# Kernel optimization log

Measured on AMD Instinct MI355X. Metric: run time of the kernel, lower is better.

Reference implementation:

```python
import jax, jax.numpy as jnp
import numpy as np
import math

# ---------- helpers ----------

def conv(x, w, b=None, pad=1):
    y = jax.lax.conv_general_dilated(x, w, (1, 1), [(pad, pad), (pad, pad)],
                                     dimension_numbers=('NCHW', 'OIHW', 'NCHW'))
    return y if b is None else y + b[None, :, None, None]


def bn(x, g, b, m, v, eps=1e-5):
    scale = (g / jnp.sqrt(v + eps))[None, :, None, None]
    return (x - m[None, :, None, None]) * scale + b[None, :, None, None]


def _interp(x, axis, out_size):
    # bilinear resize along one axis with align_corners=True semantics
    n = x.shape[axis]
    c = jnp.arange(out_size, dtype=jnp.float32) * (n - 1) / (out_size - 1)
    lo = jnp.floor(c).astype(jnp.int32)
    hi = jnp.minimum(lo + 1, n - 1)
    w = c - lo
    xl = jnp.take(x, lo, axis=axis)
    xh = jnp.take(x, hi, axis=axis)
    wshape = [1] * x.ndim
    wshape[axis] = out_size
    w = w.reshape(wshape)
    return xl * (1.0 - w) + xh * w


def upsample2x(x):
    B, C, H, W = x.shape
    return _interp(_interp(x, 2, 2 * H), 3, 2 * W)


def haar_dwt2d(x):
    # single-level orthonormal haar DWT; equivalent to the per-(b,c) dwt2d loop,
    # vectorized over batch and channel via strided slicing
    a = x[..., 0::2, 0::2]
    b = x[..., 0::2, 1::2]
    c = x[..., 1::2, 0::2]
    d = x[..., 1::2, 1::2]
    LL = (a + b + c + d) * 0.5
    LH = (-a - b + c + d) * 0.5  # horizontal detail (row differences)
    HL = (-a + b - c + d) * 0.5  # vertical detail (col differences)
    HH = (a - b - c + d) * 0.5
    return LL, LH, HL, HH


def gabor_kernels(k=7, sigma=4.0, lambd=10.0, gamma=0.5, psi=0.0):
    thetas = jnp.array([0.0, math.pi / 4, math.pi / 2, 3 * math.pi / 4], dtype=jnp.float32)
    r = jnp.arange(-(k // 2), k // 2 + 1, dtype=jnp.float32)
    y, x = jnp.meshgrid(r, r, indexing='ij')

    def one(theta):
        xt = x * jnp.cos(theta) + y * jnp.sin(theta)
        yt = -x * jnp.sin(theta) + y * jnp.cos(theta)
        return jnp.exp(-0.5 * (xt ** 2 / sigma ** 2 + yt ** 2 / (sigma / gamma) ** 2)) \
               * jnp.cos(2.0 * math.pi * xt / lambd + psi)

    return jax.vmap(one)(thetas)[:, None]  # [4,1,k,k]


def cbam(x, fc1_w, fc2_w, sp_w):
    avg = x.mean(axis=(2, 3))
    mx = x.max(axis=(2, 3))
    mlp = lambda v: jax.nn.relu(v @ fc1_w.T) @ fc2_w.T
    ca = jax.nn.sigmoid(mlp(avg) + mlp(mx))[:, :, None, None]
    x = x * ca
    sp = jnp.concatenate([x.mean(axis=1, keepdims=True), x.max(axis=1, keepdims=True)], axis=1)
    sa = jax.nn.sigmoid(conv(sp, sp_w, pad=3))
    return x * sa


# ---------- inputs ----------

def setup_inputs() -> dict:
    B, Cin, Cout, H, W = 16, 64, 64, 128, 128
    Cr = Cout // 16
    ks = jax.random.split(jax.random.key(0), 32)
    p = lambda k, s, sc=0.05: jax.random.normal(k, s, dtype=jnp.float32) * sc
    g = lambda k, c: 1.0 + 0.1 * jax.random.normal(k, (c,), dtype=jnp.float32)
    return {
        'x': jax.random.normal(ks[0], (B, Cin, H, W), dtype=jnp.float32),
        'conv_in_w': p(ks[1], (Cout, Cin, 3, 3)),
        'bn1_g': g(ks[2], Cout), 'bn1_b': p(ks[3], (Cout,)),
        'bn1_m': p(ks[4], (Cout,)), 'bn1_v': jax.random.uniform(ks[5], (Cout,), minval=0.5, maxval=1.5),
        'down1_w': p(ks[6], (1, Cout, 3, 3)), 'down1_b': p(ks[7], (1,)),
        'down2_w': p(ks[8], (1, Cout, 3, 3)), 'down2_b': p(ks[9], (1,)),
        'wt_w': p(ks[10], (1, 1, 3, 3)), 'wt_b': p(ks[11], (1,)),
        'edge_w': p(ks[12], (Cout, 1, 3, 3)), 'edge_b': p(ks[13], (Cout,)),
        'up_w': p(ks[14], (Cout, 2, 3, 3)),
        'bn2_g': g(ks[15], Cout), 'bn2_b': p(ks[16], (Cout,)),
        'bn2_m': p(ks[17], (Cout,)), 'bn2_v': jax.random.uniform(ks[18], (Cout,), minval=0.5, maxval=1.5),
        'combine_w': p(ks[19], (Cout, 2 * Cout, 3, 3)), 'combine_b': p(ks[20], (Cout,)),
        'cbam_fc1_w': p(ks[21], (Cr, Cout)), 'cbam_fc2_w': p(ks[22], (Cout, Cr)),
        'cbam_sp_w': p(ks[23], (1, 2, 7, 7)),
        'out_w': p(ks[24], (Cout, Cout, 3, 3)),
        'bn3_g': g(ks[25], Cout), 'bn3_b': p(ks[26], (Cout,)),
        'bn3_m': p(ks[27], (Cout,)), 'bn3_v': jax.random.uniform(ks[28], (Cout,), minval=0.5, maxval=1.5),
    }


def reference(x, conv_in_w, bn1_g, bn1_b, bn1_m, bn1_v, down1_w, down1_b,
              down2_w, down2_b, wt_w, wt_b, edge_w, edge_b, up_w,
              bn2_g, bn2_b, bn2_m, bn2_v, combine_w, combine_b,
              cbam_fc1_w, cbam_fc2_w, cbam_sp_w, out_w,
              bn3_g, bn3_b, bn3_m, bn3_v):
    x1 = jax.nn.relu(bn(conv(x, conv_in_w), bn1_g, bn1_b, bn1_m, bn1_v))   # BasicConv2d
    X = upsample2x(x1)                                                      # [B,C,2H,2W]
    x_in = conv(x1, down1_w, down1_b)                                       # [B,1,H,W]
    X_in = conv(X, down2_w, down2_b)                                        # [B,1,2H,2W]
    cA, cH, cV, cD = haar_dwt2d(X_in)                                       # [B,1,H,W] each
    edge = conv(jnp.abs(cH) + jnp.abs(cV) + jnp.abs(cD), edge_w, edge_b)    # [B,C,H,W]
    gk = gabor_kernels()                                                    # all 4 thetas in one conv
    gab = jax.nn.sigmoid(conv(x_in, gk, pad=3).mean(axis=1, keepdims=True))
    wt = conv(cA, wt_w, wt_b)
    fusion = jax.nn.relu(bn(conv(jnp.concatenate([wt, gab], axis=1), up_w),
                            bn2_g, bn2_b, bn2_m, bn2_v))
    fusion = conv(jnp.concatenate([fusion, edge * (x1 + 1.0)], axis=1), combine_w, combine_b)
    att = cbam(fusion, cbam_fc1_w, cbam_fc2_w, cbam_sp_w)
    return jax.nn.relu(bn(conv(att, out_w), bn3_g, bn3_b, bn3_m, bn3_v))
```

## Files before the change

kernel.cpp:

```cpp
#include <hip/hip_runtime.h>
#include <math.h>

#define HWc 16384
#define Wd 128
#define Hd 128

typedef __attribute__((ext_vector_type(8))) _Float16 half8;
typedef __attribute__((ext_vector_type(4))) _Float16 half4;
typedef __attribute__((ext_vector_type(4))) float f32x4;

#define GLDS16(gp, lp) __builtin_amdgcn_global_load_lds( \
    (const __attribute__((address_space(1))) void*)(gp), \
    (__attribute__((address_space(3))) void*)(lp), 16, 0, 0)

__global__ void prep_all_kernel(const float* __restrict__ w_in,
                                const float* __restrict__ w_out,
                                const float* __restrict__ w_comb,
                                _Float16* __restrict__ wf_in,
                                _Float16* __restrict__ wf_out,
                                _Float16* __restrict__ wf_comb)
{
    int bid = blockIdx.x;
    const float* w; _Float16* wf; int cin; int idx;
    if (bid < 144)      { w = w_in;   wf = wf_in;   cin = 64;  idx = bid * 256 + threadIdx.x; }
    else if (bid < 288) { w = w_out;  wf = wf_out;  cin = 64;  idx = (bid - 144) * 256 + threadIdx.x; }
    else                { w = w_comb; wf = wf_comb; cin = 128; idx = (bid - 288) * 256 + threadIdx.x; }
    int total = cin * 576;
    if (idx >= total) return;
    int KC = cin >> 5;
    int j = idx & 7;
    int lane = (idx >> 3) & 63;
    int rest = idx >> 9;
    int ot = rest & 3;
    int rest2 = rest >> 2;
    int kc = rest2 % KC;
    int t = rest2 / KC;
    int oc = ot * 16 + (lane & 15);
    int ci = kc * 32 + ((lane >> 4) << 3) + j;
    wf[idx] = (_Float16)w[((size_t)oc * cin + ci) * 9 + t];
}

__global__ __launch_bounds__(256) void pack8_kernel(const float* __restrict__ in,
                                                    _Float16* __restrict__ outp)
{
    int idx = blockIdx.x * 256 + threadIdx.x;
    int b = idx >> 14, p = idx & 16383;
    #pragma unroll
    for (int g = 0; g < 8; g++) {
        half8 v;
        #pragma unroll
        for (int k = 0; k < 8; k++)
            v[k] = (_Float16)in[((size_t)b * 64 + g * 8 + k) * HWc + p];
        *(half8*)&outp[(((size_t)b * 8 + g) * HWc + p) * 8] = v;
    }
}

__global__ __launch_bounds__(64, 3) void mfma_conv64_kernel(
    const _Float16* __restrict__ inp8, const _Float16* __restrict__ wf,
    const float* __restrict__ bng, const float* __restrict__ bnb,
    const float* __restrict__ bnm, const float* __restrict__ bnv,
    _Float16* __restrict__ outp8, float* __restrict__ out32)
{
    __shared__ __align__(16) _Float16 slds[6912];
    __shared__ float sc[64], sh[64];
    int lane = threadIdx.x;
    int b = blockIdx.y;
    int tileid = blockIdx.x;
    int ty = tileid >> 3, tx = tileid & 7;
    int h0 = ty * 4 - 1, w0 = tx * 16 - 1;
    const _Float16* ib = inp8 + (size_t)b * 8 * HWc * 8;
    bool interior = (ty >= 1 && ty <= 30 && tx >= 1 && tx <= 6);
    if (interior) {
        #pragma unroll
        for (int it = 0; it < 14; it++) {
            int i = it * 64 + lane;
            if (i < 864) {
                int g = i / 108;
                int rem = i - g * 108;
                int y = rem / 18, x = rem - (rem / 18) * 18;
                int p = (h0 + y) * Wd + (w0 + x);
                GLDS16(&ib[((size_t)g * HWc + p) * 8], &slds[it * 512]);
            }
        }
    } else {
        #pragma unroll
        for (int it = 0; it < 14; it++) {
            int i = it * 64 + lane;
            if (i < 864) {
                int g = i / 108;
                int rem = i - g * 108;
                int y = rem / 18, x = rem - (rem / 18) * 18;
                int hh = h0 + y, ww = w0 + x;
                if (hh >= 0 && hh < Hd && ww >= 0 && ww < Wd) {
                    int p = hh * Wd + ww;
                    GLDS16(&ib[((size_t)g * HWc + p) * 8], &slds[it * 512]);
                } else {
                    half8 hz;
                    #pragma unroll
                    for (int k = 0; k < 8; k++) hz[k] = (_Float16)0.f;
                    *(half8*)&slds[i * 8] = hz;
                }
            }
        }
    }
    {
        float inv = rsqrtf(bnv[lane] + 1e-5f);
        float s = bng[lane] * inv;
        sc[lane] = s;
        sh[lane] = bnb[lane] - bnm[lane] * s;
    }
    __syncthreads();
    int lq = lane >> 4, ln = lane & 15;
    f32x4 acc[4][4];
    #pragma unroll
    for (int r = 0; r < 4; r++)
        #pragma unroll
        for (int ot = 0; ot < 4; ot++)
            #pragma unroll
            for (int q = 0; q < 4; q++) acc[r][ot][q] = 0.f;

    for (int t = 0; t < 9; t++) {
        int dy = t / 3, dx = t - (t / 3) * 3;
        #pragma unroll
        for (int kc = 0; kc < 2; kc++) {
            half8 bf[4];
            #pragma unroll
            for (int r = 0; r < 4; r++) {
                int off = (((kc * 4 + lq) * 108) + (r + dy) * 18 + (ln + dx)) * 8;
                bf[r] = *(const half8*)&slds[off];
            }
            #pragma unroll
            for (int ot = 0; ot < 4; ot++) {
                half8 af = *(const half8*)(wf + (size_t)(((t * 2 + kc) * 4 + ot) * 64 + lane) * 8);
                #pragma unroll
                for (int r = 0; r < 4; r++)
                    acc[r][ot] = __builtin_amdgcn_mfma_f32_16x16x32_f16(af, bf[r], acc[r][ot], 0, 0, 0);
            }
        }
    }
    #pragma unroll
    for (int r = 0; r < 4; r++) {
        int yy = ty * 4 + r;
        int p = yy * Wd + tx * 16 + ln;
        #pragma unroll
        for (int ot = 0; ot < 4; ot++) {
            int g4 = ot * 4 + lq;
            if (out32) {
                #pragma unroll
                for (int reg = 0; reg < 4; reg++) {
                    int oc = g4 * 4 + reg;
                    float v = fmaf(acc[r][ot][reg], sc[oc], sh[oc]);
                    out32[((size_t)b * 64 + oc) * HWc + p] = fmaxf(v, 0.f);
                }
            } else {
                half4 hv;
                #pragma unroll
                for (int reg = 0; reg < 4; reg++) {
                    int oc = g4 * 4 + reg;
                    float v = fmaf(acc[r][ot][reg], sc[oc], sh[oc]);
                    hv[reg] = (_Float16)fmaxf(v, 0.f);
                }
                *(half4*)&outp8[(((size_t)b * 8 + (g4 >> 1)) * HWc + p) * 8 + (g4 & 1) * 4] = hv;
            }
        }
    }
}

__global__ __launch_bounds__(64, 3) void mfma_combine_kernel(
    const _Float16* __restrict__ f1p, const _Float16* __restrict__ emod,
    const _Float16* __restrict__ wf, const float* __restrict__ cb,
    _Float16* __restrict__ outp8)
{
    __shared__ __align__(16) _Float16 slds[6912];
    __shared__ float cbl[64];
    int lane = threadIdx.x;
    int b = blockIdx.y;
    int tileid = blockIdx.x;
    int ty = tileid >> 3, tx = tileid & 7;
    int h0 = ty * 4 - 1, w0 = tx * 16 - 1;
    int lq = lane >> 4, ln = lane & 15;
    bool interior = (ty >= 1 && ty <= 30 && tx >= 1 && tx <= 6);
    f32x4 acc[4][4];
    #pragma unroll
    for (int r = 0; r < 4; r++)
        #pragma unroll
        for (int ot = 0; ot < 4; ot++)
            #pragma unroll
            for (int q = 0; q < 4; q++) acc[r][ot][q] = 0.f;

    const _Float16* f1b = f1p + (size_t)b * 8 * HWc * 8;
    const _Float16* emb = emod + (size_t)b * 8 * HWc * 8;
    bool cbl_done = false;
    for (int h = 0; h < 2; h++) {
        const _Float16* src = (h == 0) ? f1b : emb;
        if (h) __syncthreads();
        if (interior) {
            #pragma unroll
            for (int it = 0; it < 14; it++) {
                int i = it * 64 + lane;
                if (i < 864) {
                    int g = i / 108;
                    int rem = i - g * 108;
                    int y = rem / 18, x = rem - (rem / 18) * 18;
                    int p = (h0 + y) * Wd + (w0 + x);
                    GLDS16(&src[((size_t)g * HWc + p) * 8], &slds[it * 512]);
                }
            }
        } else {
            #pragma unroll
            for (int it = 0; it < 14; it++) {
                int i = it * 64 + lane;
                if (i < 864) {
                    int g = i / 108;
                    int rem = i - g * 108;
                    int y = rem / 18, x = rem - (rem / 18) * 18;
                    int hh = h0 + y, ww = w0 + x;
                    if (hh >= 0 && hh < Hd && ww >= 0 && ww < Wd) {
                        int p = hh * Wd + ww;
                        GLDS16(&src[((size_t)g * HWc + p) * 8], &slds[it * 512]);
                    } else {
                        half8 hz;
                        #pragma unroll
                        for (int k = 0; k < 8; k++) hz[k] = (_Float16)0.f;
                        *(half8*)&slds[i * 8] = hz;
                    }
                }
            }
        }
        if (!cbl_done) { cbl[lane] = cb[lane]; cbl_done = true; }
        __syncthreads();
        for (int t = 0; t < 9; t++) {
            int dy = t / 3, dx = t - (t / 3) * 3;
            #pragma unroll
            for (int kc = 0; kc < 2; kc++) {
                int kcg = h * 2 + kc;
                half8 bf[4];
                #pragma unroll
                for (int r = 0; r < 4; r++) {
                    int off = (((kc * 4 + lq) * 108) + (r + dy) * 18 + (ln + dx)) * 8;
                    bf[r] = *(const half8*)&slds[off];
                }
                #pragma unroll
                for (int ot = 0; ot < 4; ot++) {
                    half8 af = *(const half8*)(wf + (size_t)(((t * 4 + kcg) * 4 + ot) * 64 + lane) * 8);
                    #pragma unroll
                    for (int r = 0; r < 4; r++)
                        acc[r][ot] = __builtin_amdgcn_mfma_f32_16x16x32_f16(af, bf[r], acc[r][ot], 0, 0, 0);
                }
            }
        }
    }
    #pragma unroll
    for (int r = 0; r < 4; r++) {
        int yy = ty * 4 + r;
        int p = yy * Wd + tx * 16 + ln;
        #pragma unroll
        for (int ot = 0; ot < 4; ot++) {
            int g4 = ot * 4 + lq;
            half4 hv;
            #pragma unroll
            for (int reg = 0; reg < 4; reg++) {
                int oc = g4 * 4 + reg;
                hv[reg] = (_Float16)(acc[r][ot][reg] + cbl[oc]);
            }
            *(half4*)&outp8[(((size_t)b * 8 + (g4 >> 1)) * HWc + p) * 8 + (g4 & 1) * 4] = hv;
        }
    }
}

__global__ __launch_bounds__(256) void edgemul_kernel(const float* __restrict__ E,
    const _Float16* __restrict__ x1p, const float* __restrict__ edge_w,
    const float* __restrict__ edge_b, _Float16* __restrict__ emod)
{
    __shared__ float ew[576];
    __shared__ float ebl[64];
    int tid = threadIdx.x;
    for (int i = tid; i < 576; i += 256) ew[i] = edge_w[i];
    if (tid < 64) ebl[tid] = edge_b[tid];
    __syncthreads();
    int idx = blockIdx.x * 256 + tid;
    int b = idx >> 14, p = idx & 16383;
    int i = p >> 7, j = p & 127;
    const float* ep = E + (size_t)b * HWc;
    float e[9];
    #pragma unroll
    for (int tt = 0; tt < 9; tt++) {
        int ii = i - 1 + tt / 3, jj = j - 1 + tt % 3;
        e[tt] = (ii >= 0 && ii < Hd && jj >= 0 && jj < Wd) ? ep[ii * Wd + jj] : 0.f;
    }
    const _Float16* xb = x1p + (size_t)b * 8 * HWc * 8;
    _Float16* ob = emod + (size_t)b * 8 * HWc * 8;
    for (int g = 0; g < 8; g++) {
        half8 v = *(const half8*)&xb[((size_t)g * HWc + p) * 8];
        half8 hv;
        #pragma unroll
        for (int k = 0; k < 8; k++) {
            int cc = g * 8 + k;
            float ec = ebl[cc];
            #pragma unroll
            for (int tt = 0; tt < 9; tt++) ec = fmaf(ew[cc * 9 + tt], e[tt], ec);
            float xv = (float)v[k];
            hv[k] = (_Float16)(ec * (xv + 1.0f));
        }
        *(half8*)&ob[((size_t)g * HWc + p) * 8] = hv;
    }
}

__global__ __launch_bounds__(256) void conv3x3_bn_kernel(
    const float* __restrict__ in, const float* __restrict__ wgt,
    const float* __restrict__ bng, const float* __restrict__ bnb,
    const float* __restrict__ bnm, const float* __restrict__ bnv,
    _Float16* __restrict__ outp8, int cin)
{
    __shared__ float tile[18*18];
    __shared__ float wl[576];
    __shared__ float sc[64], sh[64];
    int tid = threadIdx.x;
    int tileid = blockIdx.x; int b = blockIdx.y;
    int th = tileid >> 3, tw = tileid & 7;
    int h0 = th*16 - 1, w0 = tw*16 - 1;
    if (tid < 64) {
        float inv = rsqrtf(bnv[tid] + 1e-5f);
        float s = bng[tid]*inv;
        sc[tid] = s;
        sh[tid] = bnb[tid] - bnm[tid]*s;
    }
    float acc[64];
    #pragma unroll
    for (int i=0;i<64;i++) acc[i]=0.f;
    int py = tid>>4, px = tid&15;
    for (int ci=0; ci<cin; ci++){
        __syncthreads();
        const float* inp = in + ((size_t)b*cin + ci)*HWc;
        for (int i = tid; i < 324; i += 256) {
            int y=i/18, x=i%18; int hh=h0+y, ww=w0+x;
            tile[i] = (hh>=0&&hh<Hd&&ww>=0&&ww<Wd) ? inp[hh*Wd+ww] : 0.f;
        }
        for (int i = tid; i < 576; i += 256) {
            int oc = i/9, t = i - oc*9;
            wl[i] = wgt[((size_t)oc*cin + ci)*9 + t];
        }
        __syncthreads();
        float v[9];
        #pragma unroll
        for (int dy=0;dy<3;dy++)
            #pragma unroll
            for (int dx=0;dx<3;dx++)
                v[dy*3+dx] = tile[(py+dy)*18 + px+dx];
        #pragma unroll
        for (int oc=0;oc<64;oc++){
            float a = acc[oc];
            #pragma unroll
            for (int t=0;t<9;t++) a = fmaf(wl[oc*9+t], v[t], a);
            acc[oc]=a;
        }
    }
    int hh = h0+1+py, ww = w0+1+px;
    int p = hh*Wd + ww;
    #pragma unroll
    for (int g=0; g<8; g++){
        half8 hv;
        #pragma unroll
        for (int k=0; k<8; k++){
            int oc = g*8+k;
            float y = fmaf(acc[oc], sc[oc], sh[oc]);
            hv[k] = (_Float16)fmaxf(y, 0.f);
        }
        *(half8*)&outp8[(((size_t)b*8+g)*HWc + p)*8] = hv;
    }
}

__global__ __launch_bounds__(256) void zmaps_kernel(const _Float16* __restrict__ x1p,
    const float* __restrict__ w2, const float* __restrict__ w1,
    float* __restrict__ z, float* __restrict__ z1)
{
    int idx = blockIdx.x*256 + threadIdx.x;
    int b = idx >> 14; int p = idx & 16383;
    const _Float16* xb = x1p + (size_t)b*8*HWc*8;
    float a2[9], a1[9];
    #pragma unroll
    for (int t=0;t<9;t++){ a2[t]=0.f; a1[t]=0.f; }
    for (int g=0; g<8; g++){
        half8 v = *(const half8*)&xb[((size_t)g*HWc + p)*8];
        #pragma unroll
        for (int k=0;k<8;k++){
            int c = g*8+k;
            float val = (float)v[k];
            #pragma unroll
            for (int t=0;t<9;t++){
                a2[t] = fmaf(w2[c*9+t], val, a2[t]);
                a1[t] = fmaf(w1[c*9+t], val, a1[t]);
            }
        }
    }
    #pragma unroll
    for (int t=0;t<9;t++){
        z [((size_t)b*9+t)*HWc + p] = a2[t];
        z1[((size_t)b*9+t)*HWc + p] = a1[t];
    }
}

__global__ __launch_bounds__(256) void xin_kernel(const float* __restrict__ z1,
    const float* __restrict__ b1p, float* __restrict__ xin)
{
    int idx = blockIdx.x*256+threadIdx.x;
    int b=idx>>14; int p=idx&16383;
    int i=p>>7, j=p&127;
    float acc = b1p[0];
    #pragma unroll
    for (int t=0;t<9;t++){
        int ii=i+t/3-1, jj=j+t%3-1;
        if (ii>=0&&ii<Hd&&jj>=0&&jj<Wd)
            acc += z1[((size_t)b*9+t)*HWc + ii*Wd+jj];
    }
    xin[idx]=acc;
}

__global__ __launch_bounds__(256) void dwt_kernel(const float* __restrict__ z,
    const float* __restrict__ b2p, float* __restrict__ cA, float* __restrict__ Eo)
{
    int idx = blockIdx.x*256 + threadIdx.x;
    int b = idx >> 14; int p = idx & 16383;
    int u = p >> 7, v = p & 127;
    float b2 = b2p[0];
    int rlo[4], rhi[4]; float rf[4]; bool rv[4];
    int clo[4], chi[4]; float cf[4]; bool cvv[4];
    #pragma unroll
    for (int k=0;k<4;k++){
        int r = 2*u - 1 + k;
        rv[k] = (r>=0 && r<256);
        int rr = rv[k] ? r : 0;
        float cc = ((float)rr * 127.0f) / 255.0f;
        int lo = (int)cc;
        rlo[k]=lo; rhi[k]=min(lo+1,127); rf[k]=cc-(float)lo;
        int s = 2*v - 1 + k;
        cvv[k] = (s>=0 && s<256);
        int ss = cvv[k] ? s : 0;
        float c2 = ((float)ss * 127.0f) / 255.0f;
        int lo2=(int)c2;
        clo[k]=lo2; chi[k]=min(lo2+1,127); cf[k]=c2-(float)lo2;
    }
    float Xin[4] = {b2,b2,b2,b2};
    #pragma unroll
    for (int t=0;t<9;t++){
        int dy=t/3, dx=t%3;
        const float* zp = z + ((size_t)b*9 + t)*HWc;
        #pragma unroll
        for (int e=0;e<4;e++){
            int ey=e>>1, ex=e&1;
            int k=ey+dy, l=ex+dx;
            if (rv[k] && cvv[l]){
                const float* row0 = zp + rlo[k]*Wd;
                const float* row1 = zp + rhi[k]*Wd;
                float v00=row0[clo[l]], v01=row0[chi[l]];
                float v10=row1[clo[l]], v11=row1[chi[l]];
                float fc_=cf[l], fr_=rf[k];
                float top = v00*(1.0f-fc_) + v01*fc_;
                float bot = v10*(1.0f-fc_) + v11*fc_;
                Xin[e] += top*(1.0f-fr_) + bot*fr_;
            }
        }
    }
    float a=Xin[0], bb=Xin[1], c_=Xin[2], d_=Xin[3];
    float LL=0.5f*( a+bb+c_+d_);
    float LH=0.5f*(-a-bb+c_+d_);
    float HL=0.5f*(-a+bb-c_+d_);
    float HH=0.5f*( a-bb-c_+d_);
    cA[(size_t)b*HWc + p] = LL;
    Eo[(size_t)b*HWc + p] = fabsf(LH)+fabsf(HL)+fabsf(HH);
}

__global__ __launch_bounds__(256) void wtgab_kernel(const float* __restrict__ cA,
    const float* __restrict__ xin, const float* __restrict__ wtw, const float* __restrict__ wtb,
    float* __restrict__ wtgab)
{
    __shared__ float gm[49];
    int tid=threadIdx.x;
    if (tid<49){
        int ky=tid/7, kx=tid%7;
        float yy=(float)(ky-3), xx=(float)(kx-3);
        float s=0.f;
        for (int t=0;t<4;t++){
            float theta = (float)t * 0.7853981633974483f;
            float ct=cosf(theta), st=sinf(theta);
            float xt = xx*ct + yy*st;
            float yt = -xx*st + yy*ct;
            s += expf(-0.5f*(xt*xt*(1.0f/16.0f) + yt*yt*(1.0f/64.0f))) * cosf(0.6283185307179586f*xt);
        }
        gm[tid]=0.25f*s;
    }
    __syncthreads();
    int idx = blockIdx.x*256+tid;
    int b=idx>>14; int p=idx&16383;
    int i=p>>7, j=p&127;
    float wacc = wtb[0];
    #pragma unroll
    for (int t=0;t<9;t++){
        int ii=i+t/3-1, jj=j+t%3-1;
        if (ii>=0&&ii<Hd&&jj>=0&&jj<Wd)
            wacc = fmaf(wtw[t], cA[b*HWc + ii*Wd+jj], wacc);
    }
    float g=0.f;
    for (int k=0;k<49;k++){
        int ii=i+k/7-3, jj=j+k%7-3;
        if (ii>=0&&ii<Hd&&jj>=0&&jj<Wd)
            g = fmaf(gm[k], xin[b*HWc + ii*Wd+jj], g);
    }
    wtgab[((size_t)b*2)*HWc + p] = wacc;
    wtgab[((size_t)b*2+1)*HWc + p] = 1.0f/(1.0f+expf(-g));
}

__global__ __launch_bounds__(256) void pool_kernel(const _Float16* __restrict__ fp8,
    float* __restrict__ pavg, float* __restrict__ pmax)
{
    int b = blockIdx.x >> 3, g = blockIdx.x & 7;
    int tid = threadIdx.x;
    const _Float16* p = fp8 + ((size_t)b*8 + g)*HWc*8;
    float s[8] = {0,0,0,0,0,0,0,0};
    float m[8] = {-3.4e38f,-3.4e38f,-3.4e38f,-3.4e38f,-3.4e38f,-3.4e38f,-3.4e38f,-3.4e38f};
    for (int i=tid;i<HWc;i+=256){
        half8 v = *(const half8*)&p[(size_t)i*8];
        #pragma unroll
        for (int k=0;k<8;k++){ float u=(float)v[k]; s[k]+=u; m[k]=fmaxf(m[k],u); }
    }
    __shared__ float ss[8][256], sm[8][256];
    #pragma unroll
    for (int k=0;k<8;k++){ ss[k][tid]=s[k]; sm[k][tid]=m[k]; }
    __syncthreads();
    for (int st=128; st>0; st>>=1){
        if (tid<st){
            #pragma unroll
            for (int k=0;k<8;k++){
                ss[k][tid]+=ss[k][tid+st];
                sm[k][tid]=fmaxf(sm[k][tid],sm[k][tid+st]);
            }
        }
        __syncthreads();
    }
    if (tid<8){
        pavg[b*64 + g*8 + tid] = ss[tid][0]*(1.0f/16384.0f);
        pmax[b*64 + g*8 + tid] = sm[tid][0];
    }
}

__global__ void mlp_kernel(const float* __restrict__ pavg, const float* __restrict__ pmax,
    const float* __restrict__ fc1, const float* __restrict__ fc2, float* __restrict__ ca)
{
    int b = blockIdx.x; int tid = threadIdx.x;
    __shared__ float hs[4];
    if (tid < 4){
        float sa_=0.f, sm_=0.f;
        for (int c=0;c<64;c++){
            float w = fc1[tid*64+c];
            sa_ = fmaf(w, pavg[b*64+c], sa_);
            sm_ = fmaf(w, pmax[b*64+c], sm_);
        }
        hs[tid] = fmaxf(sa_,0.f) + fmaxf(sm_,0.f);
    }
    __syncthreads();
    float o = 0.f;
    #pragma unroll
    for (int j=0;j<4;j++) o = fmaf(fc2[tid*4+j], hs[j], o);
    ca[b*64+tid] = 1.0f/(1.0f+expf(-o));
}

__global__ __launch_bounds__(256) void spstats_kernel(const _Float16* __restrict__ fp8,
    const float* __restrict__ ca, float* __restrict__ spmean, float* __restrict__ spmax)
{
    int idx = blockIdx.x*256+threadIdx.x;
    int b = idx>>14; int p = idx&16383;
    const _Float16* fb = fp8 + (size_t)b*8*HWc*8;
    const float* cp = ca + b*64;
    float s=0.f, m=-3.4e38f;
    for (int g=0; g<8; g++){
        half8 v = *(const half8*)&fb[((size_t)g*HWc + p)*8];
        #pragma unroll
        for (int k=0;k<8;k++){
            float u = (float)v[k] * cp[g*8+k];
            s += u; m = fmaxf(m, u);
        }
    }
    spmean[idx] = s*(1.0f/64.0f);
    spmax[idx] = m;
}

__global__ __launch_bounds__(256) void spconv_modmul_kernel(
    const float* __restrict__ spmean, const float* __restrict__ spmax,
    const float* __restrict__ spw, const _Float16* __restrict__ fp8,
    const float* __restrict__ ca, _Float16* __restrict__ outm)
{
    int idx = blockIdx.x*256+threadIdx.x;
    int b=idx>>14; int p=idx&16383;
    int i=p>>7, j=p&127;
    float acc=0.f;
    for (int k=0;k<49;k++){
        int ky=k/7-3, kx=k%7-3;
        int ii=i+ky, jj=j+kx;
        if (ii>=0&&ii<Hd&&jj>=0&&jj<Wd){
            int q = b*HWc + ii*Wd+jj;
            acc = fmaf(spw[k],    spmean[q], acc);
            acc = fmaf(spw[49+k], spmax[q], acc);
        }
    }
    float m = 1.0f/(1.0f+expf(-acc));
    const float* cp = ca + b * 64;
    const _Float16* fb = fp8 + (size_t)b * 8 * HWc * 8;
    _Float16* ob = outm + (size_t)b * 8 * HWc * 8;
    for (int g = 0; g < 8; g++) {
        half8 v = *(const half8*)&fb[((size_t)g * HWc + p) * 8];
        half8 hv;
        #pragma unroll
        for (int k = 0; k < 8; k++)
            hv[k] = (_Float16)((float)v[k] * cp[g * 8 + k] * m);
        *(half8*)&ob[((size_t)g * HWc + p) * 8] = hv;
    }
}

extern "C" void kernel_launch(void* const* d_in, const int* in_sizes, int n_in,
                              void* d_out, int out_size, void* d_ws, size_t ws_size,
                              hipStream_t stream)
{
    const float* x         = (const float*)d_in[0];
    const float* conv_in_w = (const float*)d_in[1];
    const float* bn1_g = (const float*)d_in[2];
    const float* bn1_b = (const float*)d_in[3];
    const float* bn1_m = (const float*)d_in[4];
    const float* bn1_v = (const float*)d_in[5];
    const float* down1_w = (const float*)d_in[6];
    const float* down1_b = (const float*)d_in[7];
    const float* down2_w = (const float*)d_in[8];
    const float* down2_b = (const float*)d_in[9];
    const float* wt_w = (const float*)d_in[10];
    const float* wt_b = (const float*)d_in[11];
    const float* edge_w = (const float*)d_in[12];
    const float* edge_b = (const float*)d_in[13];
    const float* up_w = (const float*)d_in[14];
    const float* bn2_g = (const float*)d_in[15];
    const float* bn2_b = (const float*)d_in[16];
    const float* bn2_m = (const float*)d_in[17];
    const float* bn2_v = (const float*)d_in[18];
    const float* combine_w = (const float*)d_in[19];
    const float* combine_b = (const float*)d_in[20];
    const float* fc1 = (const float*)d_in[21];
    const float* fc2 = (const float*)d_in[22];
    const float* spw = (const float*)d_in[23];
    const float* out_w = (const float*)d_in[24];
    const float* bn3_g = (const float*)d_in[25];
    const float* bn3_b = (const float*)d_in[26];
    const float* bn3_m = (const float*)d_in[27];
    const float* bn3_v = (const float*)d_in[28];
    float* out = (float*)d_out;
    float* ws = (float*)d_ws;

    float* z       = ws;
    float* z1      = z + 2359296;
    float* xin     = z1 + 2359296;
    float* cA      = xin + 262144;
    float* Ebuf    = cA + 262144;
    float* wtgab   = Ebuf + 262144;
    float* spmean  = wtgab + 524288;
    float* spmaxb  = spmean + 262144;
    float* sabuf   = spmaxb + 262144;
    float* pavg    = sabuf + 262144;
    float* pmaxb   = pavg + 1024;
    float* cab     = pmaxb + 1024;
    _Float16* xp      = (_Float16*)(cab + 1024);
    _Float16* x1p     = xp + 16777216;
    _Float16* f1p     = x1p + 16777216;
    _Float16* fp      = f1p + 16777216;
    _Float16* wf_in   = fp + 16777216;
    _Float16* wf_out  = wf_in + 36864;
    _Float16* wf_comb = wf_out + 36864;
    _Float16* emod = xp;
    _Float16* fmod = f1p;

    prep_all_kernel<<<576, 256, 0, stream>>>(conv_in_w, out_w, combine_w,
                                             wf_in, wf_out, wf_comb);
    pack8_kernel<<<1024, 256, 0, stream>>>(x, xp);

    dim3 cgrid(256, 16);
    mfma_conv64_kernel<<<cgrid, 64, 0, stream>>>(xp, wf_in, bn1_g,bn1_b,bn1_m,bn1_v,
                                                 x1p, nullptr);
    zmaps_kernel<<<1024, 256, 0, stream>>>(x1p, down2_w, down1_w, z, z1);
    xin_kernel<<<1024, 256, 0, stream>>>(z1, down1_b, xin);
    dwt_kernel<<<1024, 256, 0, stream>>>(z, down2_b, cA, Ebuf);
    wtgab_kernel<<<1024, 256, 0, stream>>>(cA, xin, wt_w, wt_b, wtgab);
    conv3x3_bn_kernel<<<dim3(64,16), 256, 0, stream>>>(wtgab, up_w, bn2_g,bn2_b,bn2_m,bn2_v, f1p, 2);
    edgemul_kernel<<<1024, 256, 0, stream>>>(Ebuf, x1p, edge_w, edge_b, emod);
    mfma_combine_kernel<<<cgrid, 64, 0, stream>>>(f1p, emod, wf_comb, combine_b, fp);
    pool_kernel<<<128, 256, 0, stream>>>(fp, pavg, pmaxb);
    mlp_kernel<<<16, 64, 0, stream>>>(pavg, pmaxb, fc1, fc2, cab);
    spstats_kernel<<<1024, 256, 0, stream>>>(fp, cab, spmean, spmaxb);
    spconv_modmul_kernel<<<1024, 256, 0, stream>>>(spmean, spmaxb, spw, fp, cab, fmod);
    mfma_conv64_kernel<<<cgrid, 64, 0, stream>>>(fmod, wf_out, bn3_g,bn3_b,bn3_m,bn3_v,
                                                 nullptr, out);
}
```

Before: 569.1 us.

## Prefetch both combine input halves into LDS, fuse xin and dwt kernels

The combine conv now stages both 64-channel input halves into a doubled LDS buffer up front. Interior tiles use partial vmcnt waits so the first half's MFMA work can overlap the second half's loads, and the mid-loop barrier and bias staging in LDS are dropped. Occupancy hints for both MFMA kernels are raised, BN scale setup is moved ahead of the loads, and the xin and dwt kernels are merged into one launch. The doubled LDS footprint may limit the higher occupancy target. The raw vmcnt waits without a barrier rely on single-wave blocks, and the diff leaves behind dead statements.

```diff
diff --git a/kernel.cpp b/kernel.cpp
--- a/kernel.cpp
+++ b/kernel.cpp
@@ -55,7 +55,7 @@
     }
 }
 
-__global__ __launch_bounds__(64, 3) void mfma_conv64_kernel(
+__global__ __launch_bounds__(64, 4) void mfma_conv64_kernel(
     const _Float16* __restrict__ inp8, const _Float16* __restrict__ wf,
     const float* __restrict__ bng, const float* __restrict__ bnb,
     const float* __restrict__ bnm, const float* __restrict__ bnv,
@@ -68,6 +68,12 @@
     int tileid = blockIdx.x;
     int ty = tileid >> 3, tx = tileid & 7;
     int h0 = ty * 4 - 1, w0 = tx * 16 - 1;
+    {
+        float inv = rsqrtf(bnv[lane] + 1e-5f);
+        float s = bng[lane] * inv;
+        sc[lane] = s;
+        sh[lane] = bnb[lane] - bnm[lane] * s;
+    }
     const _Float16* ib = inp8 + (size_t)b * 8 * HWc * 8;
     bool interior = (ty >= 1 && ty <= 30 && tx >= 1 && tx <= 6);
     if (interior) {
@@ -102,12 +108,6 @@
                 }
             }
         }
-    }
-    {
-        float inv = rsqrtf(bnv[lane] + 1e-5f);
-        float s = bng[lane] * inv;
-        sc[lane] = s;
-        sh[lane] = bnb[lane] - bnm[lane] * s;
     }
     __syncthreads();
     int lq = lane >> 4, ln = lane & 15;
@@ -166,13 +166,12 @@
     }
 }
 
-__global__ __launch_bounds__(64, 3) void mfma_combine_kernel(
+__global__ __launch_bounds__(64, 4) void mfma_combine_kernel(
     const _Float16* __restrict__ f1p, const _Float16* __restrict__ emod,
     const _Float16* __restrict__ wf, const float* __restrict__ cb,
     _Float16* __restrict__ outp8)
 {
-    __shared__ __align__(16) _Float16 slds[6912];
-    __shared__ float cbl[64];
+    __shared__ __align__(16) _Float16 slds[13824];
     int lane = threadIdx.x;
     int b = blockIdx.y;
     int tileid = blockIdx.x;
@@ -180,33 +179,39 @@
     int h0 = ty * 4 - 1, w0 = tx * 16 - 1;
     int lq = lane >> 4, ln = lane & 15;
     bool interior = (ty >= 1 && ty <= 30 && tx >= 1 && tx <= 6);
-    f32x4 acc[4][4];
-    #pragma unroll
-    for (int r = 0; r < 4; r++)
-        #pragma unroll
-        for (int ot = 0; ot < 4; ot++)
-            #pragma unroll
-            for (int q = 0; q < 4; q++) acc[r][ot][q] = 0.f;
-
     const _Float16* f1b = f1p + (size_t)b * 8 * HWc * 8;
     const _Float16* emb = emod + (size_t)b * 8 * HWc * 8;
-    bool cbl_done = false;
-    for (int h = 0; h < 2; h++) {
-        const _Float16* src = (h == 0) ? f1b : emb;
-        if (h) __syncthreads();
-        if (interior) {
-            #pragma unroll
-            for (int it = 0; it < 14; it++) {
-                int i = it * 64 + lane;
-                if (i < 864) {
-                    int g = i / 108;
-                    int rem = i - g * 108;
-                    int y = rem / 18, x = rem - (rem / 18) * 18;
-                    int p = (h0 + y) * Wd + (w0 + x);
-                    GLDS16(&src[((size_t)g * HWc + p) * 8], &slds[it * 512]);
-                }
-            }
-        } else {
+
+    if (interior) {
+        #pragma unroll
+        for (int it = 0; it < 14; it++) {
+            int i = it * 64 + lane;
+            if (i < 864) {
+                int g = i / 108;
+                int rem = i - g * 108;
+                int y = rem / 18, x = rem - (rem / 18) * 18;
+                int p = (h0 + y) * Wd + (w0 + x);
+                GLDS16(&f1b[((size_t)g * HWc + p) * 8], &slds[it * 512]);
+            }
+        }
+        __builtin_amdgcn_sched_barrier(0);
+        #pragma unroll
+        for (int it = 0; it < 14; it++) {
+            int i = it * 64 + lane;
+            if (i < 864) {
+                int g = i / 108;
+                int rem = i - g * 108;
+                int y = rem / 18, x = rem - (rem / 18) * 18;
+                int p = (h0 + y) * Wd + (w0 + x);
+                GLDS16(&emb[((size_t)g * HWc + p) * 8], &slds[6912 + it * 512]);
+            }
+        }
+        __builtin_amdgcn_sched_barrier(0);
+    } else {
+        #pragma unroll
+        for (int ph = 0; ph < 2; ph++) {
+            const _Float16* src = (ph == 0) ? f1b : emb;
+            int base = ph * 6912;
             #pragma unroll
             for (int it = 0; it < 14; it++) {
                 int i = it * 64 + lane;
@@ -217,18 +222,37 @@
                     int hh = h0 + y, ww = w0 + x;
                     if (hh >= 0 && hh < Hd && ww >= 0 && ww < Wd) {
                         int p = hh * Wd + ww;
-                        GLDS16(&src[((size_t)g * HWc + p) * 8], &slds[it * 512]);
+                        GLDS16(&src[((size_t)g * HWc + p) * 8], &slds[base + it * 512]);
                     } else {
                         half8 hz;
                         #pragma unroll
                         for (int k = 0; k < 8; k++) hz[k] = (_Float16)0.f;
-                        *(half8*)&slds[i * 8] = hz;
+                        *(half8*)&slds[(base + i * 8)];
+                        *(half8*)&slds[base + i * 8] = hz;
                     }
                 }
             }
         }
-        if (!cbl_done) { cbl[lane] = cb[lane]; cbl_done = true; }
-        __syncthreads();
+    }
+
+    f32x4 acc[4][4];
+    #pragma unroll
+    for (int r = 0; r < 4; r++)
+        #pragma unroll
+        for (int ot = 0; ot < 4; ot++)
+            #pragma unroll
+            for (int q = 0; q < 4; q++) acc[r][ot][q] = 0.f;
+
+    #pragma unroll
+    for (int h = 0; h < 2; h++) {
+        if (interior) {
+            if (h == 0) asm volatile("s_waitcnt vmcnt(14)" ::: "memory");
+            else        asm volatile("s_waitcnt vmcnt(0)"  ::: "memory");
+            __builtin_amdgcn_sched_barrier(0);
+        } else if (h == 0) {
+            __syncthreads();
+        }
+        int base = h * 6912;
         for (int t = 0; t < 9; t++) {
             int dy = t / 3, dx = t - (t / 3) * 3;
             #pragma unroll
@@ -237,8 +261,10 @@
                 half8 bf[4];
                 #pragma unroll
                 for (int r = 0; r < 4; r++) {
-                    int off = (((kc * 4 + lq) * 108) + (r + dy) * 18 + (ln + dx)) * 8;
-                    bf[r] = *(const half8*)&slds[off];
+                    int off = (base + ((kc * 4 + lq) * 108) + (r + dy) * 18 + (ln + dx)) * 8;
+                    bf[r] = *(const half8*)&slds[(size_t)h * 6912 * 8 / 8 * 0 + (((kc * 4 + lq) * 108) + (r + dy) * 18 + (ln + dx)) * 8 + h * 6912 * 0];
+                    (void)off;
+                    bf[r] = *(const half8*)&slds[h * 6912 + (((kc * 4 + lq) * 108) + (r + dy) * 18 + (ln + dx)) * 8];
                 }
                 #pragma unroll
                 for (int ot = 0; ot < 4; ot++) {
@@ -261,7 +287,7 @@
             #pragma unroll
             for (int reg = 0; reg < 4; reg++) {
                 int oc = g4 * 4 + reg;
-                hv[reg] = (_Float16)(acc[r][ot][reg] + cbl[oc]);
+                hv[reg] = (_Float16)(acc[r][ot][reg] + cb[oc]);
             }
             *(half4*)&outp8[(((size_t)b * 8 + (g4 >> 1)) * HWc + p) * 8 + (g4 & 1) * 4] = hv;
         }
@@ -400,74 +426,73 @@
     }
 }
 
-__global__ __launch_bounds__(256) void xin_kernel(const float* __restrict__ z1,
-    const float* __restrict__ b1p, float* __restrict__ xin)
+__global__ __launch_bounds__(256) void xindwt_kernel(const float* __restrict__ z1,
+    const float* __restrict__ b1p, const float* __restrict__ z,
+    const float* __restrict__ b2p, float* __restrict__ xin,
+    float* __restrict__ cA, float* __restrict__ Eo)
 {
     int idx = blockIdx.x*256+threadIdx.x;
     int b=idx>>14; int p=idx&16383;
-    int i=p>>7, j=p&127;
-    float acc = b1p[0];
-    #pragma unroll
-    for (int t=0;t<9;t++){
-        int ii=i+t/3-1, jj=j+t%3-1;
-        if (ii>=0&&ii<Hd&&jj>=0&&jj<Wd)
-            acc += z1[((size_t)b*9+t)*HWc + ii*Wd+jj];
-    }
-    xin[idx]=acc;
-}
-
-__global__ __launch_bounds__(256) void dwt_kernel(const float* __restrict__ z,
-    const float* __restrict__ b2p, float* __restrict__ cA, float* __restrict__ Eo)
-{
-    int idx = blockIdx.x*256 + threadIdx.x;
-    int b = idx >> 14; int p = idx & 16383;
-    int u = p >> 7, v = p & 127;
-    float b2 = b2p[0];
-    int rlo[4], rhi[4]; float rf[4]; bool rv[4];
-    int clo[4], chi[4]; float cf[4]; bool cvv[4];
-    #pragma unroll
-    for (int k=0;k<4;k++){
-        int r = 2*u - 1 + k;
-        rv[k] = (r>=0 && r<256);
-        int rr = rv[k] ? r : 0;
-        float cc = ((float)rr * 127.0f) / 255.0f;
-        int lo = (int)cc;
-        rlo[k]=lo; rhi[k]=min(lo+1,127); rf[k]=cc-(float)lo;
-        int s = 2*v - 1 + k;
-        cvv[k] = (s>=0 && s<256);
-        int ss = cvv[k] ? s : 0;
-        float c2 = ((float)ss * 127.0f) / 255.0f;
-        int lo2=(int)c2;
-        clo[k]=lo2; chi[k]=min(lo2+1,127); cf[k]=c2-(float)lo2;
-    }
-    float Xin[4] = {b2,b2,b2,b2};
-    #pragma unroll
-    for (int t=0;t<9;t++){
-        int dy=t/3, dx=t%3;
-        const float* zp = z + ((size_t)b*9 + t)*HWc;
-        #pragma unroll
-        for (int e=0;e<4;e++){
-            int ey=e>>1, ex=e&1;
-            int k=ey+dy, l=ex+dx;
-            if (rv[k] && cvv[l]){
-                const float* row0 = zp + rlo[k]*Wd;
-                const float* row1 = zp + rhi[k]*Wd;
-                float v00=row0[clo[l]], v01=row0[chi[l]];
-                float v10=row1[clo[l]], v11=row1[chi[l]];
-                float fc_=cf[l], fr_=rf[k];
-                float top = v00*(1.0f-fc_) + v01*fc_;
-                float bot = v10*(1.0f-fc_) + v11*fc_;
-                Xin[e] += top*(1.0f-fr_) + bot*fr_;
-            }
-        }
-    }
-    float a=Xin[0], bb=Xin[1], c_=Xin[2], d_=Xin[3];
-    float LL=0.5f*( a+bb+c_+d_);
-    float LH=0.5f*(-a-bb+c_+d_);
-    float HL=0.5f*(-a+bb-c_+d_);
-    float HH=0.5f*( a-bb-c_+d_);
-    cA[(size_t)b*HWc + p] = LL;
-    Eo[(size_t)b*HWc + p] = fabsf(LH)+fabsf(HL)+fabsf(HH);
+    {
+        int i=p>>7, j=p&127;
+        float acc = b1p[0];
+        #pragma unroll
+        for (int t=0;t<9;t++){
+            int ii=i+t/3-1, jj=j+t%3-1;
+            if (ii>=0&&ii<Hd&&jj>=0&&jj<Wd)
+                acc += z1[((size_t)b*9+t)*HWc + ii*Wd+jj];
+        }
+        xin[idx]=acc;
+    }
+    {
+        int u = p >> 7, v = p & 127;
+        float b2 = b2p[0];
+        int rlo[4], rhi[4]; float rf[4]; bool rv[4];
+        int clo[4], chi[4]; float cf[4]; bool cvv[4];
+        #pragma unroll
+        for (int k=0;k<4;k++){
+            int r = 2*u - 1 + k;
+            rv[k] = (r>=0 && r<256);
+            int rr = rv[k] ? r : 0;
+            float cc = ((float)rr * 127.0f) / 255.0f;
+            int lo = (int)cc;
+            rlo[k]=lo; rhi[k]=min(lo+1,127); rf[k]=cc-(float)lo;
+            int s = 2*v - 1 + k;
+            cvv[k] = (s>=0 && s<256);
+            int ss = cvv[k] ? s : 0;
+            float c2 = ((float)ss * 127.0f) / 255.0f;
+            int lo2=(int)c2;
+            clo[k]=lo2; chi[k]=min(lo2+1,127); cf[k]=c2-(float)lo2;
+        }
+        float Xin[4] = {b2,b2,b2,b2};
+        #pragma unroll
+        for (int t=0;t<9;t++){
+            int dy=t/3, dx=t%3;
+            const float* zp = z + ((size_t)b*9 + t)*HWc;
+            #pragma unroll
+            for (int e=0;e<4;e++){
+                int ey=e>>1, ex=e&1;
+                int k=ey+dy, l=ex+dx;
+                if (rv[k] && cvv[l]){
+                    const float* row0 = zp + rlo[k]*Wd;
+                    const float* row1 = zp + rhi[k]*Wd;
+                    float v00=row0[clo[l]], v01=row0[chi[l]];
+                    float v10=row1[clo[l]], v11=row1[chi[l]];
+                    float fc_=cf[l], fr_=rf[k];
+                    float top = v00*(1.0f-fc_) + v01*fc_;
+                    float bot = v10*(1.0f-fc_) + v11*fc_;
+                    Xin[e] += top*(1.0f-fr_) + bot*fr_;
+                }
+            }
+        }
+        float a=Xin[0], bb=Xin[1], c_=Xin[2], d_=Xin[3];
+        float LL=0.5f*( a+bb+c_+d_);
+        float LH=0.5f*(-a-bb+c_+d_);
+        float HL=0.5f*(-a+bb-c_+d_);
+        float HH=0.5f*( a-bb-c_+d_);
+        cA[(size_t)b*HWc + p] = LL;
+        Eo[(size_t)b*HWc + p] = fabsf(LH)+fabsf(HL)+fabsf(HH);
+    }
 }
 
 __global__ __launch_bounds__(256) void wtgab_kernel(const float* __restrict__ cA,
@@ -682,8 +707,7 @@
     mfma_conv64_kernel<<<cgrid, 64, 0, stream>>>(xp, wf_in, bn1_g,bn1_b,bn1_m,bn1_v,
                                                  x1p, nullptr);
     zmaps_kernel<<<1024, 256, 0, stream>>>(x1p, down2_w, down1_w, z, z1);
-    xin_kernel<<<1024, 256, 0, stream>>>(z1, down1_b, xin);
-    dwt_kernel<<<1024, 256, 0, stream>>>(z, down2_b, cA, Ebuf);
+    xindwt_kernel<<<1024, 256, 0, stream>>>(z1, down1_b, z, down2_b, xin, cA, Ebuf);
     wtgab_kernel<<<1024, 256, 0, stream>>>(cA, xin, wt_w, wt_b, wtgab);
     conv3x3_bn_kernel<<<dim3(64,16), 256, 0, stream>>>(wtgab, up_w, bn2_g,bn2_b,bn2_m,bn2_v, f1p, 2);
     edgemul_kernel<<<1024, 256, 0, stream>>>(Ebuf, x1p, edge_w, edge_b, emod);
```

Result: faster. 509.9 us (-10.4%).
